# Optimization experiments

Hardware: AMD Instinct MI355X
Metric: run time of the kernel (lower is better)

Reference implementation:

```python
import jax, jax.numpy as jnp
import numpy as np

N = 50000   # nodes
E = 800000  # edges (before self loops)
NEG_SLOPE = 0.2
EPS_BN = 1e-5
EPS_SM = 1e-16  # PyG softmax denominator epsilon


def gat_conv(x, src, dst, W, att_src, att_dst, bias, heads, ch):
    n = x.shape[0]
    xh = (x @ W).reshape(n, heads, ch)                       # [N,H,C]
    a_src = jnp.sum(xh * att_src, axis=-1)                   # [N,H]
    a_dst = jnp.sum(xh * att_dst, axis=-1)                   # [N,H]
    e = a_src[src] + a_dst[dst]                              # [E,H]
    e = jax.nn.leaky_relu(e, NEG_SLOPE)
    m = jax.ops.segment_max(e, dst, num_segments=n)          # segment softmax
    ex = jnp.exp(e - m[dst])
    denom = jax.ops.segment_sum(ex, dst, num_segments=n)
    alpha = ex / (denom[dst] + EPS_SM)                       # [E,H]
    msg = alpha[:, :, None] * xh[src]                        # [E,H,C]
    out = jax.ops.segment_sum(msg, dst, num_segments=n)      # [N,H,C]
    return out.reshape(n, heads * ch) + bias


def batch_norm(x, gamma, beta):
    mu = jnp.mean(x, axis=0)
    var = jnp.mean((x - mu) ** 2, axis=0)
    return (x - mu) * jax.lax.rsqrt(var + EPS_BN) * gamma + beta


def setup_inputs() -> dict:
    key = jax.random.key(0)
    ks = jax.random.split(key, 16)
    d = {}
    d['x'] = jax.random.normal(ks[0], (N, 128), jnp.float32)
    d['edge_index'] = jax.random.randint(ks[1], (2, E), 0, N, dtype=jnp.int64)
    d['W1'] = jax.random.normal(ks[2], (128, 256), jnp.float32) * 0.1
    d['as1'] = jax.random.normal(ks[3], (2, 128), jnp.float32) * 0.1
    d['ad1'] = jax.random.normal(ks[4], (2, 128), jnp.float32) * 0.1
    d['b1'] = jax.random.normal(ks[5], (256,), jnp.float32) * 0.1
    d['g1'] = jnp.ones((256,), jnp.float32)
    d['be1'] = jnp.zeros((256,), jnp.float32)
    d['W2'] = jax.random.normal(ks[6], (256, 128), jnp.float32) * 0.1
    d['as2'] = jax.random.normal(ks[7], (2, 64), jnp.float32) * 0.1
    d['ad2'] = jax.random.normal(ks[8], (2, 64), jnp.float32) * 0.1
    d['b2'] = jax.random.normal(ks[9], (128,), jnp.float32) * 0.1
    d['g2'] = jnp.ones((128,), jnp.float32)
    d['be2'] = jnp.zeros((128,), jnp.float32)
    d['W3'] = jax.random.normal(ks[10], (128, 128), jnp.float32) * 0.1
    d['as3'] = jax.random.normal(ks[11], (2, 64), jnp.float32) * 0.1
    d['ad3'] = jax.random.normal(ks[12], (2, 64), jnp.float32) * 0.1
    d['b3'] = jax.random.normal(ks[13], (128,), jnp.float32) * 0.1
    d['lw'] = jax.random.normal(ks[14], (128, 64), jnp.float32) * 0.1
    d['lb'] = jnp.zeros((64,), jnp.float32)
    return d


def reference(x, edge_index, W1, as1, ad1, b1, g1, be1,
              W2, as2, ad2, b2, g2, be2,
              W3, as3, ad3, b3, lw, lb):
    # add self loops (PyG GATConv default add_self_loops=True)
    loops = jnp.arange(N, dtype=edge_index.dtype)
    src = jnp.concatenate([edge_index[0], loops])
    dst = jnp.concatenate([edge_index[1], loops])

    h = jax.nn.relu(gat_conv(x, src, dst, W1, as1, ad1, b1, 2, 128))   # [N,256]
    h = batch_norm(h, g1, be1)
    h = jax.nn.relu(gat_conv(h, src, dst, W2, as2, ad2, b2, 2, 64))    # [N,128]
    h = batch_norm(h, g2, be2)
    h = jax.nn.relu(gat_conv(h, src, dst, W3, as3, ad3, b3, 2, 64))    # [N,128]
    return h @ lw + lb                                                 # [N,64]
```

## Files before the change

### kernel.cpp

```cpp
#include <hip/hip_runtime.h>
#include <hip/hip_bf16.h>

#define NEG_SLOPE 0.2f
#define EPS_BN 1e-5f
#define EPS_SM 1e-16f

typedef __bf16 bf16x8 __attribute__((ext_vector_type(8)));
typedef __bf16 bf16x4 __attribute__((ext_vector_type(4)));
typedef float floatx4 __attribute__((ext_vector_type(4)));

__device__ __forceinline__ float leaky(float x) { return x > 0.f ? x : NEG_SLOPE * x; }

__global__ void k_detect(const int* __restrict__ ei, int* __restrict__ cnt, int e) {
    int i = threadIdx.x + blockIdx.x * blockDim.x;
    if (i < 1024 && 2 * i + 1 < 2 * e) {
        if (ei[2 * i + 1] != 0) atomicAdd(cnt, 1);
    }
}

__global__ void k_hist(const int* __restrict__ ei, const int* __restrict__ cnt,
                       int* __restrict__ deg, int* __restrict__ rnk, int e) {
    int g = threadIdx.x + blockIdx.x * blockDim.x;
    if (g >= e) return;
    bool is64 = (*cnt) < 512;
    int d = is64 ? ei[2 * (e + g)] : ei[e + g];
    rnk[g] = atomicAdd(&deg[d], 1);
}

__global__ __launch_bounds__(1024) void k_scan1(const int* __restrict__ deg,
                                                int* __restrict__ excl,
                                                int* __restrict__ bsum, int n) {
    __shared__ int sm[1024];
    int tid = threadIdx.x;
    int g = blockIdx.x * 1024 + tid;
    int v = (g < n) ? deg[g] : 0;
    sm[tid] = v;
    __syncthreads();
    for (int off = 1; off < 1024; off <<= 1) {
        int t = (tid >= off) ? sm[tid - off] : 0;
        __syncthreads();
        sm[tid] += t;
        __syncthreads();
    }
    if (g < n) excl[g] = sm[tid] - v;
    if (tid == 1023) bsum[blockIdx.x] = sm[1023];
}

__global__ void k_scan3(const int* __restrict__ excl, const int* __restrict__ bsum,
                        int* __restrict__ rowptr, int n, int e) {
    __shared__ int pref;
    int g = threadIdx.x + blockIdx.x * blockDim.x;
    if (threadIdx.x == 0) {
        int chunk = (blockIdx.x * blockDim.x) >> 10;
        int acc = 0;
        for (int i = 0; i < chunk; ++i) acc += bsum[i];
        pref = acc;
    }
    __syncthreads();
    if (g < n) rowptr[g] = excl[g] + pref;
    if (g == 0) rowptr[n] = e;
}

__global__ void k_scatter(const int* __restrict__ ei, const int* __restrict__ cnt,
                          const int* __restrict__ rowptr, const int* __restrict__ rnk,
                          int* __restrict__ col, int e) {
    int g = threadIdx.x + blockIdx.x * blockDim.x;
    if (g >= e) return;
    bool is64 = (*cnt) < 512;
    int s = is64 ? ei[2 * g] : ei[g];
    int d = is64 ? ei[2 * (e + g)] : ei[e + g];
    col[rowptr[d] + rnk[g]] = s;
}

__global__ void k_wconv(const float* __restrict__ W1, __bf16* __restrict__ Wb1,
                        const float* __restrict__ W2, __bf16* __restrict__ Wb2,
                        const float* __restrict__ W3, __bf16* __restrict__ Wb3) {
    int idx = threadIdx.x + blockIdx.x * blockDim.x;
    if (idx < 32768) {
        int mm = idx >> 7, kk = idx & 127;
        Wb1[idx] = (__bf16)W1[(size_t)kk * 256 + mm];
    } else if (idx < 65536) {
        int i2 = idx - 32768;
        int mm = i2 >> 8, kk = i2 & 255;
        Wb2[i2] = (__bf16)W2[(size_t)kk * 128 + mm];
    } else if (idx < 81920) {
        int i3 = idx - 65536;
        int mm = i3 >> 7, kk = i3 & 127;
        Wb3[i3] = (__bf16)W3[(size_t)kk * 128 + mm];
    }
}

template <int K, int LC, bool BF16IN>
__global__ __launch_bounds__(256) void k_gemm(const void* __restrict__ Ain,
                                              const __bf16* __restrict__ Bt,
                                              __bf16* __restrict__ Cb, int n, int M,
                                              const float* __restrict__ bnsums,
                                              const float* __restrict__ gam,
                                              const float* __restrict__ bet,
                                              const float* __restrict__ att_s,
                                              const float* __restrict__ att_d,
                                              float* __restrict__ asrc,
                                              float* __restrict__ adst) {
    __shared__ __align__(16) __bf16 As[128][72];
    __shared__ __align__(16) __bf16 Bs[128][72];
    __shared__ float sc_lds[K], sh_lds[K];
    const int row0 = blockIdx.y * 128, col0 = blockIdx.x * 128;
    const int lane = threadIdx.x & 63, w = threadIdx.x >> 6;
    const int m = lane & 15, quad = lane >> 4;

    if (bnsums) {
        for (int c = threadIdx.x; c < K; c += 256) {
            float mean = bnsums[c] / n;
            float var = bnsums[256 + c] / n - mean * mean;
            float sc = gam[c] * rsqrtf(var + EPS_BN);
            sc_lds[c] = sc;
            sh_lds[c] = bet[c] - mean * sc;
        }
        __syncthreads();
    }

    floatx4 acc[2][8];
#pragma unroll
    for (int i = 0; i < 2; ++i)
#pragma unroll
        for (int j = 0; j < 8; ++j) acc[i][j] = (floatx4)0.f;

    const int sr = threadIdx.x >> 1;
    const int sk = (threadIdx.x & 1) * 32;

    for (int kc = 0; kc < K; kc += 64) {
        {
            int grow = row0 + sr;
            if (grow < n) {
                if (BF16IN) {
                    const __bf16* p = (const __bf16*)Ain + (size_t)grow * K + kc + sk;
#pragma unroll
                    for (int q = 0; q < 4; ++q) {
                        bf16x8 vv = *reinterpret_cast<const bf16x8*>(p + q * 8);
                        if (bnsums) {
                            int c = kc + sk + q * 8;
                            bf16x8 r;
#pragma unroll
                            for (int e2 = 0; e2 < 8; ++e2)
                                r[e2] = (__bf16)((float)vv[e2] * sc_lds[c + e2] + sh_lds[c + e2]);
                            vv = r;
                        }
                        *reinterpret_cast<bf16x8*>(&As[sr][sk + q * 8]) = vv;
                    }
                } else {
                    const float* p = (const float*)Ain + (size_t)grow * K + kc + sk;
#pragma unroll
                    for (int q = 0; q < 8; ++q) {
                        float4 v = *reinterpret_cast<const float4*>(p + q * 4);
                        bf16x4 cv = {(__bf16)v.x, (__bf16)v.y, (__bf16)v.z, (__bf16)v.w};
                        *reinterpret_cast<bf16x4*>(&As[sr][sk + q * 4]) = cv;
                    }
                }
            } else {
#pragma unroll
                for (int q = 0; q < 4; ++q)
                    *reinterpret_cast<bf16x8*>(&As[sr][sk + q * 8]) = (bf16x8)(__bf16)0.f;
            }
        }
        {
            const __bf16* p = Bt + (size_t)(col0 + sr) * K + kc + sk;
#pragma unroll
            for (int q = 0; q < 4; ++q)
                *reinterpret_cast<bf16x8*>(&Bs[sr][sk + q * 8]) =
                    *reinterpret_cast<const bf16x8*>(p + q * 8);
        }
        __syncthreads();
#pragma unroll
        for (int ks = 0; ks < 64; ks += 32) {
            bf16x8 a0 = *reinterpret_cast<const bf16x8*>(&As[w * 32 + m][ks + quad * 8]);
            bf16x8 a1 = *reinterpret_cast<const bf16x8*>(&As[w * 32 + 16 + m][ks + quad * 8]);
#pragma unroll
            for (int nt = 0; nt < 8; ++nt) {
                bf16x8 b = *reinterpret_cast<const bf16x8*>(&Bs[nt * 16 + m][ks + quad * 8]);
                acc[0][nt] = __builtin_amdgcn_mfma_f32_16x16x32_bf16(a0, b, acc[0][nt], 0, 0, 0);
                acc[1][nt] = __builtin_amdgcn_mfma_f32_16x16x32_bf16(a1, b, acc[1][nt], 0, 0, 0);
            }
        }
        __syncthreads();
    }
#pragma unroll
    for (int mt = 0; mt < 2; ++mt)
#pragma unroll
        for (int nt = 0; nt < 8; ++nt)
#pragma unroll
            for (int r = 0; r < 4; ++r) {
                int row = row0 + w * 32 + mt * 16 + quad * 4 + r;
                if (row < n) Cb[(size_t)row * M + col0 + nt * 16 + m] = (__bf16)acc[mt][nt][r];
            }
    {
        float asv[8], adv[8];
#pragma unroll
        for (int nt = 0; nt < 8; ++nt) {
            int c = col0 + nt * 16 + m;
            asv[nt] = att_s[c];
            adv[nt] = att_d[c];
        }
#pragma unroll
        for (int mt = 0; mt < 2; ++mt)
#pragma unroll
            for (int r = 0; r < 4; ++r) {
                int row = row0 + w * 32 + mt * 16 + quad * 4 + r;
                if (LC == 7) {
                    float pa = 0.f, pb = 0.f;
#pragma unroll
                    for (int nt = 0; nt < 8; ++nt) {
                        float v = acc[mt][nt][r];
                        pa += v * asv[nt];
                        pb += v * adv[nt];
                    }
#pragma unroll
                    for (int off = 1; off <= 8; off <<= 1) {
                        pa += __shfl_xor(pa, off);
                        pb += __shfl_xor(pb, off);
                    }
                    if (m == 0 && row < n) {
                        int h = (col0 >> 7) & 1;
                        atomicAdd(asrc + 2 * row + h, pa);
                        atomicAdd(adst + 2 * row + h, pb);
                    }
                } else {
                    float p00 = 0.f, p01 = 0.f, p10 = 0.f, p11 = 0.f;
#pragma unroll
                    for (int nt = 0; nt < 8; ++nt) {
                        float v = acc[mt][nt][r];
                        if (nt < 4) { p00 += v * asv[nt]; p10 += v * adv[nt]; }
                        else        { p01 += v * asv[nt]; p11 += v * adv[nt]; }
                    }
#pragma unroll
                    for (int off = 1; off <= 8; off <<= 1) {
                        p00 += __shfl_xor(p00, off);
                        p01 += __shfl_xor(p01, off);
                        p10 += __shfl_xor(p10, off);
                        p11 += __shfl_xor(p11, off);
                    }
                    if (m == 0 && row < n) {
                        atomicAdd(asrc + 2 * row + 0, p00);
                        atomicAdd(asrc + 2 * row + 1, p01);
                        atomicAdd(adst + 2 * row + 0, p10);
                        atomicAdd(adst + 2 * row + 1, p11);
                    }
                }
            }
    }
}

__global__ __launch_bounds__(256) void k_lin(const float* __restrict__ A,
                                             const float* __restrict__ lw,
                                             const float* __restrict__ lb,
                                             float* __restrict__ out, int n) {
    __shared__ __align__(16) __bf16 Ahi[64][136];
    __shared__ __align__(16) __bf16 Alo[64][136];
    __shared__ __align__(16) __bf16 Bhi[64][136];
    const int row0 = blockIdx.x * 64;
    const int lane = threadIdx.x & 63, w = threadIdx.x >> 6;
    const int m = lane & 15, quad = lane >> 4;
    floatx4 acc[4];
#pragma unroll
    for (int i = 0; i < 4; ++i) acc[i] = (floatx4)0.f;
    {
        int sr = threadIdx.x >> 2, sk0 = (threadIdx.x & 3) * 32;
        int grow = row0 + sr;
#pragma unroll
        for (int q = 0; q < 8; ++q) {
            float4 v = make_float4(0.f, 0.f, 0.f, 0.f);
            if (grow < n) v = *reinterpret_cast<const float4*>(A + (size_t)grow * 128 + sk0 + q * 4);
            float vv[4] = {v.x, v.y, v.z, v.w};
#pragma unroll
            for (int i = 0; i < 4; ++i) {
                __bf16 h = (__bf16)vv[i];
                Ahi[sr][sk0 + q * 4 + i] = h;
                Alo[sr][sk0 + q * 4 + i] = (__bf16)(vv[i] - (float)h);
            }
        }
    }
    {
        int k0 = threadIdx.x >> 1, m0 = (threadIdx.x & 1) * 32;
#pragma unroll
        for (int q = 0; q < 8; ++q) {
            float4 v = *reinterpret_cast<const float4*>(lw + (size_t)k0 * 64 + m0 + q * 4);
            float vv[4] = {v.x, v.y, v.z, v.w};
#pragma unroll
            for (int i = 0; i < 4; ++i) Bhi[m0 + q * 4 + i][k0] = (__bf16)vv[i];
        }
    }
    __syncthreads();
#pragma unroll
    for (int ks = 0; ks < 128; ks += 32) {
        bf16x8 ah = *reinterpret_cast<const bf16x8*>(&Ahi[w * 16 + m][ks + quad * 8]);
        bf16x8 al = *reinterpret_cast<const bf16x8*>(&Alo[w * 16 + m][ks + quad * 8]);
#pragma unroll
        for (int nt = 0; nt < 4; ++nt) {
            bf16x8 bh = *reinterpret_cast<const bf16x8*>(&Bhi[nt * 16 + m][ks + quad * 8]);
            acc[nt] = __builtin_amdgcn_mfma_f32_16x16x32_bf16(ah, bh, acc[nt], 0, 0, 0);
            acc[nt] = __builtin_amdgcn_mfma_f32_16x16x32_bf16(al, bh, acc[nt], 0, 0, 0);
        }
    }
#pragma unroll
    for (int nt = 0; nt < 4; ++nt)
#pragma unroll
        for (int r = 0; r < 4; ++r) {
            int row = row0 + w * 16 + quad * 4 + r;
            int c = nt * 16 + m;
            if (row < n) out[(size_t)row * 64 + c] = acc[nt][r] + lb[c];
        }
}

template <int C, bool OUTBF16>
__global__ __launch_bounds__(256) void k_agg(const __bf16* __restrict__ xh,
                                             const float* __restrict__ asrc,
                                             const float* __restrict__ adst,
                                             const int* __restrict__ rowptr,
                                             const int* __restrict__ col,
                                             const float* __restrict__ bias,
                                             void* __restrict__ outv, int n) {
    constexpr int F = 2 * C;
    constexpr int G = F / 8;
    constexpr int NG = 64 / G;
    constexpr int GSH = (G == 32) ? 5 : 4;
    __shared__ float4 slots[4][72];
    const int widx = threadIdx.x >> 6;
    const int node = blockIdx.x * 4 + widx;
    const int lane = threadIdx.x & 63;
    if (node >= n) return;
    const int t = lane & (G - 1);
    const int g = lane >> GSH;
    const bool h1 = (t * 8) >= C;
    if (lane < 8) slots[widx][64 + lane] = make_float4(0.f, 0.f, 0.f, 0.f);
    const int beg = rowptr[node];
    const int deg = rowptr[node + 1] - beg;
    const float2 adv = *reinterpret_cast<const float2*>(adst + 2 * node);
    const float2 asv = *reinterpret_cast<const float2*>(asrc + 2 * node);
    const float es0 = leaky(asv.x + adv.x), es1 = leaky(asv.y + adv.y);
    float acc[8] = {};
    float d0 = 0.f, d1 = 0.f;

    for (int base = 0; base < deg; base += 64) {
        const int cnt = min(64, deg - base);
        float4 sv = make_float4(0.f, 0.f, 0.f, 0.f);
        if (lane < cnt) {
            int s = col[beg + base + lane];
            float2 av = *reinterpret_cast<const float2*>(asrc + 2 * s);
            float w0 = __expf(leaky(av.x + adv.x));
            float w1 = __expf(leaky(av.y + adv.y));
            d0 += w0; d1 += w1;
            sv = make_float4(__int_as_float(s * (F * 2)), w0, w1, 0.f);
        }
        slots[widx][lane] = sv;
        for (int j = g; j < cnt; j += 2 * NG) {
            float4 s0 = slots[widx][j];
            float4 s1 = slots[widx][j + NG];
            const char* p0 = (const char*)xh + (unsigned)__float_as_int(s0.x);
            const char* p1 = (const char*)xh + (unsigned)__float_as_int(s1.x);
            bf16x8 v0 = *reinterpret_cast<const bf16x8*>(p0 + t * 16);
            bf16x8 v1 = *reinterpret_cast<const bf16x8*>(p1 + t * 16);
            float w0 = h1 ? s0.z : s0.y;
            float w1 = h1 ? s1.z : s1.y;
#pragma unroll
            for (int q = 0; q < 8; ++q) acc[q] += w0 * (float)v0[q] + w1 * (float)v1[q];
        }
    }
#pragma unroll
    for (int off = 1; off <= 32; off <<= 1) {
        d0 += __shfl_xor(d0, off);
        d1 += __shfl_xor(d1, off);
    }
#pragma unroll
    for (int q = 0; q < 8; ++q) {
#pragma unroll
        for (int off = G; off < 64; off <<= 1) acc[q] += __shfl_xor(acc[q], off);
    }
    float exs0 = __expf(es0), exs1 = __expf(es1);
    d0 += exs0; d1 += exs1;
    {
        float ws = h1 ? exs1 : exs0;
        const __bf16* p = xh + (size_t)node * F + t * 8;
        bf16x8 v = *reinterpret_cast<const bf16x8*>(p);
#pragma unroll
        for (int q = 0; q < 8; ++q) acc[q] += ws * (float)v[q];
    }
    float inv = 1.0f / ((h1 ? d1 : d0) + EPS_SM);
    float o[8];
#pragma unroll
    for (int q = 0; q < 8; ++q) o[q] = fmaxf(acc[q] * inv + bias[t * 8 + q], 0.f);
    if (g == 0) {
        if constexpr (OUTBF16) {
            __bf16* po = (__bf16*)outv + (size_t)node * F + t * 8;
            bf16x8 st;
#pragma unroll
            for (int q = 0; q < 8; ++q) st[q] = (__bf16)o[q];
            *reinterpret_cast<bf16x8*>(po) = st;
        } else {
            float* po = (float*)outv + (size_t)node * F + t * 8;
            *reinterpret_cast<float4*>(po) = make_float4(o[0], o[1], o[2], o[3]);
            *reinterpret_cast<float4*>(po + 4) = make_float4(o[4], o[5], o[6], o[7]);
        }
    }
}

template <typename T>
__global__ void k_bn_stats(const T* __restrict__ x, float* __restrict__ sums,
                           float* __restrict__ sqs, int n, int f) {
    int c = threadIdx.x;
    float s = 0.f, q = 0.f;
    for (int r = blockIdx.x; r < n; r += gridDim.x) {
        float v = (float)x[(size_t)r * f + c];
        s += v; q += v * v;
    }
    atomicAdd(&sums[c], s);
    atomicAdd(&sqs[c], q);
}

extern "C" void kernel_launch(void* const* d_in, const int* in_sizes, int n_in,
                              void* d_out, int out_size, void* d_ws, size_t ws_size,
                              hipStream_t stream) {
    const float* x   = (const float*)d_in[0];
    const int*   ei  = (const int*)d_in[1];
    const float* W1  = (const float*)d_in[2];
    const float* as1 = (const float*)d_in[3];
    const float* ad1 = (const float*)d_in[4];
    const float* b1  = (const float*)d_in[5];
    const float* g1  = (const float*)d_in[6];
    const float* be1 = (const float*)d_in[7];
    const float* W2  = (const float*)d_in[8];
    const float* as2 = (const float*)d_in[9];
    const float* ad2 = (const float*)d_in[10];
    const float* b2  = (const float*)d_in[11];
    const float* g2  = (const float*)d_in[12];
    const float* be2 = (const float*)d_in[13];
    const float* W3  = (const float*)d_in[14];
    const float* as3 = (const float*)d_in[15];
    const float* ad3 = (const float*)d_in[16];
    const float* b3  = (const float*)d_in[17];
    const float* lw  = (const float*)d_in[18];
    const float* lb  = (const float*)d_in[19];
    float* outp = (float*)d_out;

    const int n = in_sizes[0] / 128;
    const int e = in_sizes[1] / 2;

    char* w = (char*)d_ws;
    size_t off = 0;
    auto alloc = [&](size_t bytes) -> void* {
        void* p = w + off;
        off += (bytes + 255) & ~(size_t)255;
        return p;
    };
    __bf16* xhb = (__bf16*)alloc((size_t)n * 256 * 2);
    __bf16* h1b = (__bf16*)alloc((size_t)n * 256 * 2);
    __bf16* h2b = (__bf16*)alloc((size_t)n * 128 * 2);
    float*  h3f = (float*)alloc((size_t)n * 128 * 4);
    int* excl   = (int*)alloc((size_t)n * 4);
    int* rowptr = (int*)alloc((size_t)(n + 1) * 4);
    int* colb   = (int*)alloc((size_t)e * 4);
    int* rnk    = (int*)alloc((size_t)e * 4);
    int* bsum   = (int*)alloc(64 * 4);
    __bf16* Wb1 = (__bf16*)alloc(256 * 128 * 2);
    __bf16* Wb2 = (__bf16*)alloc(128 * 256 * 2);
    __bf16* Wb3 = (__bf16*)alloc(128 * 128 * 2);
    char* zb_begin = (char*)(w + off);
    int* deg    = (int*)alloc((size_t)n * 4);
    float* bn1  = (float*)alloc(512 * 4);
    float* bn2  = (float*)alloc(512 * 4);
    int* dcnt   = (int*)alloc(256);
    float* as1p = (float*)alloc((size_t)n * 2 * 4);
    float* ad1p = (float*)alloc((size_t)n * 2 * 4);
    float* as2p = (float*)alloc((size_t)n * 2 * 4);
    float* ad2p = (float*)alloc((size_t)n * 2 * 4);
    float* as3p = (float*)alloc((size_t)n * 2 * 4);
    float* ad3p = (float*)alloc((size_t)n * 2 * 4);
    char* zb_end = (char*)(w + off);

    const int nb1 = (n + 1023) / 1024;

    hipMemsetAsync(zb_begin, 0, (size_t)(zb_end - zb_begin), stream);

    k_detect<<<4, 256, 0, stream>>>(ei, dcnt, e);
    k_hist<<<(e + 255) / 256, 256, 0, stream>>>(ei, dcnt, deg, rnk, e);
    k_scan1<<<nb1, 1024, 0, stream>>>(deg, excl, bsum, n);
    k_scan3<<<(n + 255) / 256, 256, 0, stream>>>(excl, bsum, rowptr, n, e);
    k_scatter<<<(e + 255) / 256, 256, 0, stream>>>(ei, dcnt, rowptr, rnk, colb, e);
    k_wconv<<<(81920 + 255) / 256, 256, 0, stream>>>(W1, Wb1, W2, Wb2, W3, Wb3);

    const int nwb = (n + 3) / 4;
    const int nrow = (n + 127) / 128;

    k_gemm<128, 7, false><<<dim3(2, nrow), 256, 0, stream>>>(
        x, Wb1, xhb, n, 256, nullptr, nullptr, nullptr, as1, ad1, as1p, ad1p);
    k_agg<128, true><<<nwb, 256, 0, stream>>>(xhb, as1p, ad1p, rowptr, colb, b1, h1b, n);
    k_bn_stats<__bf16><<<256, 256, 0, stream>>>(h1b, bn1, bn1 + 256, n, 256);

    k_gemm<256, 6, true><<<dim3(1, nrow), 256, 0, stream>>>(
        h1b, Wb2, xhb, n, 128, bn1, g1, be1, as2, ad2, as2p, ad2p);
    k_agg<64, true><<<nwb, 256, 0, stream>>>(xhb, as2p, ad2p, rowptr, colb, b2, h2b, n);
    k_bn_stats<__bf16><<<256, 128, 0, stream>>>(h2b, bn2, bn2 + 256, n, 128);

    k_gemm<128, 6, true><<<dim3(1, nrow), 256, 0, stream>>>(
        h2b, Wb3, xhb, n, 128, bn2, g2, be2, as3, ad3, as3p, ad3p);
    k_agg<64, false><<<nwb, 256, 0, stream>>>(xhb, as3p, ad3p, rowptr, colb, b3, h3f, n);

    k_lin<<<(n + 63) / 64, 256, 0, stream>>>(h3f, lw, lb, outp, n);
}
```

Measured before the change: 477.0 us.

## Fuse batch-norm statistics into aggregation, merge weight conversion into scan, unroll gather

```diff
diff --git a/kernel.cpp b/kernel.cpp
--- a/kernel.cpp
+++ b/kernel.cpp
@@ -27,9 +27,28 @@
     rnk[g] = atomicAdd(&deg[d], 1);
 }
 
-__global__ __launch_bounds__(1024) void k_scan1(const int* __restrict__ deg,
-                                                int* __restrict__ excl,
-                                                int* __restrict__ bsum, int n) {
+__global__ __launch_bounds__(1024) void k_scan1_wconv(
+    const int* __restrict__ deg, int* __restrict__ excl, int* __restrict__ bsum,
+    int n, int nb1,
+    const float* __restrict__ W1, __bf16* __restrict__ Wb1,
+    const float* __restrict__ W2, __bf16* __restrict__ Wb2,
+    const float* __restrict__ W3, __bf16* __restrict__ Wb3) {
+    if ((int)blockIdx.x >= nb1) {
+        int idx = ((int)blockIdx.x - nb1) * 1024 + threadIdx.x;
+        if (idx < 32768) {
+            int mm = idx >> 7, kk = idx & 127;
+            Wb1[idx] = (__bf16)W1[(size_t)kk * 256 + mm];
+        } else if (idx < 65536) {
+            int i2 = idx - 32768;
+            int mm = i2 >> 8, kk = i2 & 255;
+            Wb2[i2] = (__bf16)W2[(size_t)kk * 128 + mm];
+        } else if (idx < 81920) {
+            int i3 = idx - 65536;
+            int mm = i3 >> 7, kk = i3 & 127;
+            Wb3[i3] = (__bf16)W3[(size_t)kk * 128 + mm];
+        }
+        return;
+    }
     __shared__ int sm[1024];
     int tid = threadIdx.x;
     int g = blockIdx.x * 1024 + tid;
@@ -70,24 +89,6 @@
     int s = is64 ? ei[2 * g] : ei[g];
     int d = is64 ? ei[2 * (e + g)] : ei[e + g];
     col[rowptr[d] + rnk[g]] = s;
-}
-
-__global__ void k_wconv(const float* __restrict__ W1, __bf16* __restrict__ Wb1,
-                        const float* __restrict__ W2, __bf16* __restrict__ Wb2,
-                        const float* __restrict__ W3, __bf16* __restrict__ Wb3) {
-    int idx = threadIdx.x + blockIdx.x * blockDim.x;
-    if (idx < 32768) {
-        int mm = idx >> 7, kk = idx & 127;
-        Wb1[idx] = (__bf16)W1[(size_t)kk * 256 + mm];
-    } else if (idx < 65536) {
-        int i2 = idx - 32768;
-        int mm = i2 >> 8, kk = i2 & 255;
-        Wb2[i2] = (__bf16)W2[(size_t)kk * 128 + mm];
-    } else if (idx < 81920) {
-        int i3 = idx - 65536;
-        int mm = i3 >> 7, kk = i3 & 127;
-        Wb3[i3] = (__bf16)W3[(size_t)kk * 128 + mm];
-    }
 }
 
 template <int K, int LC, bool BF16IN>
@@ -317,102 +318,114 @@
                                              const int* __restrict__ rowptr,
                                              const int* __restrict__ col,
                                              const float* __restrict__ bias,
-                                             void* __restrict__ outv, int n) {
+                                             void* __restrict__ outv,
+                                             float* __restrict__ bn, int n) {
     constexpr int F = 2 * C;
     constexpr int G = F / 8;
     constexpr int NG = 64 / G;
     constexpr int GSH = (G == 32) ? 5 : 4;
-    __shared__ float4 slots[4][72];
+    __shared__ float4 slots[4][80];
+    __shared__ float bns[2][OUTBF16 ? F : 1];
     const int widx = threadIdx.x >> 6;
     const int node = blockIdx.x * 4 + widx;
     const int lane = threadIdx.x & 63;
-    if (node >= n) return;
     const int t = lane & (G - 1);
     const int g = lane >> GSH;
     const bool h1 = (t * 8) >= C;
-    if (lane < 8) slots[widx][64 + lane] = make_float4(0.f, 0.f, 0.f, 0.f);
-    const int beg = rowptr[node];
-    const int deg = rowptr[node + 1] - beg;
-    const float2 adv = *reinterpret_cast<const float2*>(adst + 2 * node);
-    const float2 asv = *reinterpret_cast<const float2*>(asrc + 2 * node);
-    const float es0 = leaky(asv.x + adv.x), es1 = leaky(asv.y + adv.y);
-    float acc[8] = {};
-    float d0 = 0.f, d1 = 0.f;
-
-    for (int base = 0; base < deg; base += 64) {
-        const int cnt = min(64, deg - base);
-        float4 sv = make_float4(0.f, 0.f, 0.f, 0.f);
-        if (lane < cnt) {
-            int s = col[beg + base + lane];
-            float2 av = *reinterpret_cast<const float2*>(asrc + 2 * s);
-            float w0 = __expf(leaky(av.x + adv.x));
-            float w1 = __expf(leaky(av.y + adv.y));
-            d0 += w0; d1 += w1;
-            sv = make_float4(__int_as_float(s * (F * 2)), w0, w1, 0.f);
-        }
-        slots[widx][lane] = sv;
-        for (int j = g; j < cnt; j += 2 * NG) {
-            float4 s0 = slots[widx][j];
-            float4 s1 = slots[widx][j + NG];
-            const char* p0 = (const char*)xh + (unsigned)__float_as_int(s0.x);
-            const char* p1 = (const char*)xh + (unsigned)__float_as_int(s1.x);
-            bf16x8 v0 = *reinterpret_cast<const bf16x8*>(p0 + t * 16);
-            bf16x8 v1 = *reinterpret_cast<const bf16x8*>(p1 + t * 16);
-            float w0 = h1 ? s0.z : s0.y;
-            float w1 = h1 ? s1.z : s1.y;
-#pragma unroll
-            for (int q = 0; q < 8; ++q) acc[q] += w0 * (float)v0[q] + w1 * (float)v1[q];
-        }
-    }
-#pragma unroll
-    for (int off = 1; off <= 32; off <<= 1) {
-        d0 += __shfl_xor(d0, off);
-        d1 += __shfl_xor(d1, off);
-    }
-#pragma unroll
-    for (int q = 0; q < 8; ++q) {
-#pragma unroll
-        for (int off = G; off < 64; off <<= 1) acc[q] += __shfl_xor(acc[q], off);
-    }
-    float exs0 = __expf(es0), exs1 = __expf(es1);
-    d0 += exs0; d1 += exs1;
-    {
-        float ws = h1 ? exs1 : exs0;
-        const __bf16* p = xh + (size_t)node * F + t * 8;
-        bf16x8 v = *reinterpret_cast<const bf16x8*>(p);
-#pragma unroll
-        for (int q = 0; q < 8; ++q) acc[q] += ws * (float)v[q];
-    }
-    float inv = 1.0f / ((h1 ? d1 : d0) + EPS_SM);
+    const bool active = node < n;
+    if (lane >= 48) slots[widx][lane + 16] = make_float4(0.f, 0.f, 0.f, 0.f);
     float o[8];
-#pragma unroll
-    for (int q = 0; q < 8; ++q) o[q] = fmaxf(acc[q] * inv + bias[t * 8 + q], 0.f);
-    if (g == 0) {
-        if constexpr (OUTBF16) {
-            __bf16* po = (__bf16*)outv + (size_t)node * F + t * 8;
-            bf16x8 st;
-#pragma unroll
-            for (int q = 0; q < 8; ++q) st[q] = (__bf16)o[q];
-            *reinterpret_cast<bf16x8*>(po) = st;
-        } else {
-            float* po = (float*)outv + (size_t)node * F + t * 8;
-            *reinterpret_cast<float4*>(po) = make_float4(o[0], o[1], o[2], o[3]);
-            *reinterpret_cast<float4*>(po + 4) = make_float4(o[4], o[5], o[6], o[7]);
-        }
-    }
-}
-
-template <typename T>
-__global__ void k_bn_stats(const T* __restrict__ x, float* __restrict__ sums,
-                           float* __restrict__ sqs, int n, int f) {
-    int c = threadIdx.x;
-    float s = 0.f, q = 0.f;
-    for (int r = blockIdx.x; r < n; r += gridDim.x) {
-        float v = (float)x[(size_t)r * f + c];
-        s += v; q += v * v;
-    }
-    atomicAdd(&sums[c], s);
-    atomicAdd(&sqs[c], q);
+    if (active) {
+        const int beg = rowptr[node];
+        const int deg = rowptr[node + 1] - beg;
+        const float2 adv = *reinterpret_cast<const float2*>(adst + 2 * node);
+        const float2 asv = *reinterpret_cast<const float2*>(asrc + 2 * node);
+        const float es0 = leaky(asv.x + adv.x), es1 = leaky(asv.y + adv.y);
+        float acc[8] = {};
+        float d0 = 0.f, d1 = 0.f;
+        for (int base = 0; base < deg; base += 64) {
+            const int cnt = min(64, deg - base);
+            float4 sv = make_float4(0.f, 0.f, 0.f, 0.f);
+            if (lane < cnt) {
+                int s = col[beg + base + lane];
+                float2 av = *reinterpret_cast<const float2*>(asrc + 2 * s);
+                float w0 = __expf(leaky(av.x + adv.x));
+                float w1 = __expf(leaky(av.y + adv.y));
+                d0 += w0; d1 += w1;
+                sv = make_float4(__int_as_float(s * (F * 2)), w0, w1, 0.f);
+            }
+            slots[widx][lane] = sv;
+            for (int j = g; j < cnt; j += 4 * NG) {
+                float4 s0 = slots[widx][j];
+                float4 s1 = slots[widx][j + NG];
+                float4 s2 = slots[widx][j + 2 * NG];
+                float4 s3 = slots[widx][j + 3 * NG];
+                const char* xb = (const char*)xh;
+                bf16x8 v0 = *reinterpret_cast<const bf16x8*>(xb + (unsigned)__float_as_int(s0.x) + t * 16);
+                bf16x8 v1 = *reinterpret_cast<const bf16x8*>(xb + (unsigned)__float_as_int(s1.x) + t * 16);
+                bf16x8 v2 = *reinterpret_cast<const bf16x8*>(xb + (unsigned)__float_as_int(s2.x) + t * 16);
+                bf16x8 v3 = *reinterpret_cast<const bf16x8*>(xb + (unsigned)__float_as_int(s3.x) + t * 16);
+                float w0 = h1 ? s0.z : s0.y;
+                float w1 = h1 ? s1.z : s1.y;
+                float w2 = h1 ? s2.z : s2.y;
+                float w3 = h1 ? s3.z : s3.y;
+#pragma unroll
+                for (int q = 0; q < 8; ++q)
+                    acc[q] += w0 * (float)v0[q] + w1 * (float)v1[q] +
+                              w2 * (float)v2[q] + w3 * (float)v3[q];
+            }
+        }
+#pragma unroll
+        for (int off = 1; off <= 32; off <<= 1) {
+            d0 += __shfl_xor(d0, off);
+            d1 += __shfl_xor(d1, off);
+        }
+#pragma unroll
+        for (int q = 0; q < 8; ++q) {
+#pragma unroll
+            for (int off = G; off < 64; off <<= 1) acc[q] += __shfl_xor(acc[q], off);
+        }
+        float exs0 = __expf(es0), exs1 = __expf(es1);
+        d0 += exs0; d1 += exs1;
+        {
+            float ws = h1 ? exs1 : exs0;
+            bf16x8 v = *reinterpret_cast<const bf16x8*>(xh + (size_t)node * F + t * 8);
+#pragma unroll
+            for (int q = 0; q < 8; ++q) acc[q] += ws * (float)v[q];
+        }
+        float inv = 1.0f / ((h1 ? d1 : d0) + EPS_SM);
+#pragma unroll
+        for (int q = 0; q < 8; ++q) o[q] = fmaxf(acc[q] * inv + bias[t * 8 + q], 0.f);
+        if (g == 0) {
+            if constexpr (OUTBF16) {
+                __bf16* po = (__bf16*)outv + (size_t)node * F + t * 8;
+                bf16x8 st;
+#pragma unroll
+                for (int q = 0; q < 8; ++q) st[q] = (__bf16)o[q];
+                *reinterpret_cast<bf16x8*>(po) = st;
+            } else {
+                float* po = (float*)outv + (size_t)node * F + t * 8;
+                *reinterpret_cast<float4*>(po) = make_float4(o[0], o[1], o[2], o[3]);
+                *reinterpret_cast<float4*>(po + 4) = make_float4(o[4], o[5], o[6], o[7]);
+            }
+        }
+    }
+    if constexpr (OUTBF16) {
+        for (int c = threadIdx.x; c < 2 * F; c += 256) (&bns[0][0])[c] = 0.f;
+        __syncthreads();
+        if (active && g == 0) {
+#pragma unroll
+            for (int q = 0; q < 8; ++q) {
+                atomicAdd(&bns[0][t * 8 + q], o[q]);
+                atomicAdd(&bns[1][t * 8 + q], o[q] * o[q]);
+            }
+        }
+        __syncthreads();
+        for (int c = threadIdx.x; c < F; c += 256) {
+            atomicAdd(bn + c, bns[0][c]);
+            atomicAdd(bn + 256 + c, bns[1][c]);
+        }
+    }
 }
 
 extern "C" void kernel_launch(void* const* d_in, const int* in_sizes, int n_in,
@@ -481,27 +494,25 @@
 
     k_detect<<<4, 256, 0, stream>>>(ei, dcnt, e);
     k_hist<<<(e + 255) / 256, 256, 0, stream>>>(ei, dcnt, deg, rnk, e);
-    k_scan1<<<nb1, 1024, 0, stream>>>(deg, excl, bsum, n);
+    k_scan1_wconv<<<nb1 + 80, 1024, 0, stream>>>(deg, excl, bsum, n, nb1,
+                                                 W1, Wb1, W2, Wb2, W3, Wb3);
     k_scan3<<<(n + 255) / 256, 256, 0, stream>>>(excl, bsum, rowptr, n, e);
     k_scatter<<<(e + 255) / 256, 256, 0, stream>>>(ei, dcnt, rowptr, rnk, colb, e);
-    k_wconv<<<(81920 + 255) / 256, 256, 0, stream>>>(W1, Wb1, W2, Wb2, W3, Wb3);
 
     const int nwb = (n + 3) / 4;
     const int nrow = (n + 127) / 128;
 
     k_gemm<128, 7, false><<<dim3(2, nrow), 256, 0, stream>>>(
         x, Wb1, xhb, n, 256, nullptr, nullptr, nullptr, as1, ad1, as1p, ad1p);
-    k_agg<128, true><<<nwb, 256, 0, stream>>>(xhb, as1p, ad1p, rowptr, colb, b1, h1b, n);
-    k_bn_stats<__bf16><<<256, 256, 0, stream>>>(h1b, bn1, bn1 + 256, n, 256);
+    k_agg<128, true><<<nwb, 256, 0, stream>>>(xhb, as1p, ad1p, rowptr, colb, b1, h1b, bn1, n);
 
     k_gemm<256, 6, true><<<dim3(1, nrow), 256, 0, stream>>>(
         h1b, Wb2, xhb, n, 128, bn1, g1, be1, as2, ad2, as2p, ad2p);
-    k_agg<64, true><<<nwb, 256, 0, stream>>>(xhb, as2p, ad2p, rowptr, colb, b2, h2b, n);
-    k_bn_stats<__bf16><<<256, 128, 0, stream>>>(h2b, bn2, bn2 + 256, n, 128);
+    k_agg<64, true><<<nwb, 256, 0, stream>>>(xhb, as2p, ad2p, rowptr, colb, b2, h2b, bn2, n);
 
     k_gemm<128, 6, true><<<dim3(1, nrow), 256, 0, stream>>>(
         h2b, Wb3, xhb, n, 128, bn2, g2, be2, as3, ad3, as3p, ad3p);
-    k_agg<64, false><<<nwb, 256, 0, stream>>>(xhb, as3p, ad3p, rowptr, colb, b3, h3f, n);
+    k_agg<64, false><<<nwb, 256, 0, stream>>>(xhb, as3p, ad3p, rowptr, colb, b3, h3f, nullptr, n);
 
     k_lin<<<(n + 63) / 64, 256, 0, stream>>>(h3f, lw, lb, outp, n);
 }
```

Measured after the change: 921.5 us. 1.93x slower.
